# Performance work log

Measured on AMD Instinct MI355X. Metric: run time of the kernel, lower is better.

Reference implementation:

```python
import jax, jax.numpy as jnp
import numpy as np

L = 10   # lattice side (hardcoded self.length)
K = 3    # kernel_size -> half_k = 1 wrap padding
FN = 4   # filter_num
B = 262144


def setup_inputs() -> dict:
    key = jax.random.key(0)
    k1, k2, k3, k4, k5 = jax.random.split(key, 5)
    v = jax.random.normal(k1, (B, L * L), dtype=jnp.float32)
    # torch default init scale ~ 1/sqrt(fan_in)
    conv_w = jax.random.normal(k2, (FN, 1, K, K), dtype=jnp.float32) / 3.0
    conv_b = jax.random.normal(k3, (FN,), dtype=jnp.float32) * 0.1
    deconv_w = jax.random.normal(k4, (FN, 1, 2, 2), dtype=jnp.float32) / 4.0
    deconv_b = jax.random.normal(k5, (1,), dtype=jnp.float32) * 0.1
    data = jnp.zeros((1,), dtype=jnp.int32)  # unused positional arg of log_psi
    return {"v": v, "conv_w": conv_w, "conv_b": conv_b,
            "deconv_w": deconv_w, "deconv_b": deconv_b, "data": data}


def _log_psi(v, conv_w, conv_b, deconv_w, deconv_b):
    b = v.shape[0]
    x = v.reshape(b, 1, L, L)
    # handmade_padding == periodic (wrap) pad of width half_k=1 on both spatial axes
    x = jnp.pad(x, ((0, 0), (0, 0), (1, 1), (1, 1)), mode="wrap")  # [B,1,12,12]
    # Conv2d(1, FN, 3), VALID -> [B,FN,10,10]
    y = jax.lax.conv_general_dilated(
        x, conv_w, window_strides=(1, 1), padding="VALID",
        dimension_numbers=("NCHW", "OIHW", "NCHW"))
    y = y + conv_b[None, :, None, None]
    # MaxPool2d(2,2): non-overlapping 2x2 -> [B,FN,5,5]
    y = y.reshape(b, FN, L // 2, 2, L // 2, 2).max(axis=(3, 5))
    # ConvTranspose2d(FN,1,kernel=2,stride=2): each input pixel -> disjoint 2x2 block
    # torch weight layout [in=FN, out=1, 2, 2]
    z = jnp.einsum("bcij,cokl->boikjl", y, deconv_w).reshape(b, 1, L, L)
    z = z + deconv_b[None, :, None, None]
    sign_z = jnp.sign(z)
    abs_z = z * sign_z
    sign_prod = sign_z.reshape(b, -1).prod(axis=1)        # scalar per sample
    log_sum = jnp.log(abs_z).reshape(b, -1).sum(axis=1)   # scalar per sample
    return sign_prod, log_sum


def reference(v, conv_w, conv_b, deconv_w, deconv_b, data):
    return _log_psi(v, conv_w, conv_b, deconv_w, deconv_b)
```

## Files before the change

### kernel.cpp

```cpp
#include <hip/hip_runtime.h>
#include <math.h>


#define SREAD(x) __int_as_float(__builtin_amdgcn_readfirstlane(__float_as_int(x)))

__device__ __forceinline__ void gload16(const float* g, float* l) {
    __builtin_amdgcn_global_load_lds(
        (const __attribute__((address_space(1))) void*)g,
        (__attribute__((address_space(3))) void*)l, 16, 0, 0);
}
__device__ __forceinline__ void gload4(const float* g, float* l) {
    __builtin_amdgcn_global_load_lds(
        (const __attribute__((address_space(1))) void*)g,
        (__attribute__((address_space(3))) void*)l, 4, 0, 0);
}

__global__ __launch_bounds__(64) void CNN2D_37495064494620_kernel(
    const float* __restrict__ v,
    const float* __restrict__ cw,
    const float* __restrict__ cb,
    const float* __restrict__ dw,
    const float* __restrict__ db,
    float* __restrict__ out,
    int B)
{
    const int l  = threadIdx.x;
    const int q  = l & 1;
    const int sl = l >> 1;

    __shared__ __align__(16) float sm[3200];

    const float* gbase = v + (size_t)blockIdx.x * 3200;
    #pragma unroll
    for (int k = 0; k < 12; ++k)
        gload16(gbase + k * 256 + l * 4, &sm[k * 256]);
    #pragma unroll
    for (int k = 0; k < 2; ++k)
        gload4(gbase + 3072 + k * 64 + l, &sm[3072 + k * 64]);

    float W[4][9];
    #pragma unroll
    for (int f = 0; f < 4; ++f)
        #pragma unroll
        for (int t = 0; t < 9; ++t)
            W[f][t] = SREAD(cw[f * 9 + t]);
    float Cb[4];
    #pragma unroll
    for (int f = 0; f < 4; ++f) Cb[f] = SREAD(cb[f]);
    float Dw[4][4];
    #pragma unroll
    for (int f = 0; f < 4; ++f)
        #pragma unroll
        for (int t = 0; t < 4; ++t)
            Dw[f][t] = SREAD(dw[f * 4 + t]);
    const float Db = SREAD(db[0]);

    __syncthreads();

    const float* my = sm + sl * 100;

    unsigned sbits = 0u;
    float l2 = 0.0f;

    #pragma unroll
    for (int i = 0; i < 5; ++i) {
        const int r1 = 2 * i + q;
        const int r0 = (i == 0) ? (q ? 0 : 9) : (2 * i - 1 + q);
        const int r2 = (i == 4) ? (q ? 0 : 9) : (2 * i + 1 + q);

        float R[3][10];
        #pragma unroll
        for (int t = 0; t < 5; ++t) {
            float2 x0 = *(const float2*)(my + r0 * 10 + 2 * t);
            float2 x1 = *(const float2*)(my + r1 * 10 + 2 * t);
            float2 x2 = *(const float2*)(my + r2 * 10 + 2 * t);
            R[0][2 * t] = x0.x; R[0][2 * t + 1] = x0.y;
            R[1][2 * t] = x1.x; R[1][2 * t + 1] = x1.y;
            R[2][2 * t] = x2.x; R[2][2 * t + 1] = x2.y;
        }

        float M[5][4];
        #pragma unroll
        for (int j = 0; j < 5; ++j) {
            float a0[4], a1[4];
            #pragma unroll
            for (int f = 0; f < 4; ++f) { a0[f] = Cb[f]; a1[f] = Cb[f]; }
            #pragma unroll
            for (int kr = 0; kr < 3; ++kr) {
                #pragma unroll
                for (int kc = 0; kc < 3; ++kc) {
                    const int cc0 = (2 * j + kc + 9) % 10;
                    const int cc1 = (2 * j + 1 + kc + 9) % 10;
                    const float x0 = R[kr][cc0];
                    const float x1 = R[kr][cc1];
                    const int t = kr * 3 + kc;
                    #pragma unroll
                    for (int f = 0; f < 4; ++f) {
                        a0[f] = fmaf(x0, W[f][t], a0[f]);
                        a1[f] = fmaf(x1, W[f][t], a1[f]);
                    }
                }
            }
            #pragma unroll
            for (int f = 0; f < 4; ++f)
                M[j][f] = fmaxf(a0[f], a1[f]);
        }

        float P[5][4];
        #pragma unroll
        for (int j = 0; j < 5; ++j)
            #pragma unroll
            for (int f = 0; f < 4; ++f)
                P[j][f] = fmaxf(M[j][f], __shfl_xor(M[j][f], 1));

        #pragma unroll
        for (int j = 0; j < 5; ++j) {
            float z[4];
            #pragma unroll
            for (int kl = 0; kl < 4; ++kl) {
                float zz = Db;
                #pragma unroll
                for (int f = 0; f < 4; ++f)
                    zz = fmaf(P[j][f], Dw[f][kl], zz);
                z[kl] = zz;
                sbits ^= __float_as_uint(zz);
            }
            l2 += __log2f(fabsf(z[0] * z[1])) + __log2f(fabsf(z[2] * z[3]));
        }
    }

    const int s = blockIdx.x * 32 + sl;
    const float val = q ? (l2 * 0.69314718055994531f)
                        : ((sbits & 0x80000000u) ? -1.0f : 1.0f);
    out[q * B + s] = val;
}

extern "C" void kernel_launch(void* const* d_in, const int* in_sizes, int n_in,
                              void* d_out, int out_size, void* d_ws, size_t ws_size,
                              hipStream_t stream) {
    const float* v  = (const float*)d_in[0];
    const float* cw = (const float*)d_in[1];
    const float* cb = (const float*)d_in[2];
    const float* dw = (const float*)d_in[3];
    const float* db = (const float*)d_in[4];
    float* out = (float*)d_out;

    const int B = in_sizes[0] / 100;
    const int grid = B / 32;
    CNN2D_37495064494620_kernel<<<grid, 64, 0, stream>>>(v, cw, cb, dw, db, out, B);
}
```

Measured before the change: 169.3 us.

## Pack conv FMAs into v2f, split deconv across lane pairs, use DPP swaps

The conv accumulation now uses two-wide float vectors so the compiler can emit packed FMA instructions. The transposed-conv work is split between the two lanes of each pair, so each lane computes only two of the four outputs, and the partial sums and sign bits are combined at the end. Lane-pair shuffles are replaced with DPP quad-permute moves. The block grows from 64 to 256 threads covering 128 samples, which adds LDS per block (about 50KB) and may limit occupancy.

```diff
diff --git a/kernel.cpp b/kernel.cpp
--- a/kernel.cpp
+++ b/kernel.cpp
@@ -2,7 +2,16 @@
 #include <math.h>
 
 
+typedef float v2f __attribute__((ext_vector_type(2)));
+
 #define SREAD(x) __int_as_float(__builtin_amdgcn_readfirstlane(__float_as_int(x)))
+
+__device__ __forceinline__ float dpp_swap1_f(float x) {
+    return __int_as_float(__builtin_amdgcn_mov_dpp(__float_as_int(x), 0xB1, 0xF, 0xF, true));
+}
+__device__ __forceinline__ unsigned dpp_swap1_u(unsigned x) {
+    return (unsigned)__builtin_amdgcn_mov_dpp((int)x, 0xB1, 0xF, 0xF, true);
+}
 
 __device__ __forceinline__ void gload16(const float* g, float* l) {
     __builtin_amdgcn_global_load_lds(
@@ -15,7 +24,7 @@
         (__attribute__((address_space(3))) void*)l, 4, 0, 0);
 }
 
-__global__ __launch_bounds__(64) void CNN2D_37495064494620_kernel(
+__global__ __launch_bounds__(256) void CNN2D_37495064494620_kernel(
     const float* __restrict__ v,
     const float* __restrict__ cw,
     const float* __restrict__ cb,
@@ -24,29 +33,35 @@
     float* __restrict__ out,
     int B)
 {
-    const int l  = threadIdx.x;
-    const int q  = l & 1;
-    const int sl = l >> 1;
+    const int tid = threadIdx.x;
+    const int q   = tid & 1;
+    const int sl  = tid >> 1;
 
-    __shared__ __align__(16) float sm[3200];
+    __shared__ __align__(16) float sm[12800];
 
-    const float* gbase = v + (size_t)blockIdx.x * 3200;
+    const float* gbase = v + (size_t)blockIdx.x * 12800;
+    const int widx = tid >> 6;
     #pragma unroll
     for (int k = 0; k < 12; ++k)
-        gload16(gbase + k * 256 + l * 4, &sm[k * 256]);
+        gload16(gbase + k * 1024 + tid * 4, &sm[k * 1024 + widx * 256]);
     #pragma unroll
     for (int k = 0; k < 2; ++k)
-        gload4(gbase + 3072 + k * 64 + l, &sm[3072 + k * 64]);
+        gload4(gbase + 12288 + k * 256 + tid, &sm[12288 + k * 256 + widx * 64]);
 
-    float W[4][9];
+    float Wf[4][9];
     #pragma unroll
     for (int f = 0; f < 4; ++f)
         #pragma unroll
         for (int t = 0; t < 9; ++t)
-            W[f][t] = SREAD(cw[f * 9 + t]);
-    float Cb[4];
+            Wf[f][t] = SREAD(cw[f * 9 + t]);
+    v2f W2[9][2];
     #pragma unroll
-    for (int f = 0; f < 4; ++f) Cb[f] = SREAD(cb[f]);
+    for (int t = 0; t < 9; ++t) {
+        W2[t][0] = (v2f){Wf[0][t], Wf[1][t]};
+        W2[t][1] = (v2f){Wf[2][t], Wf[3][t]};
+    }
+    const v2f Cb2[2] = { (v2f){SREAD(cb[0]), SREAD(cb[1])},
+                         (v2f){SREAD(cb[2]), SREAD(cb[3])} };
     float Dw[4][4];
     #pragma unroll
     for (int f = 0; f < 4; ++f)
@@ -54,6 +69,11 @@
         for (int t = 0; t < 4; ++t)
             Dw[f][t] = SREAD(dw[f * 4 + t]);
     const float Db = SREAD(db[0]);
+
+    v2f Dq[4];
+    #pragma unroll
+    for (int f = 0; f < 4; ++f)
+        Dq[f] = (v2f){ q ? Dw[f][2] : Dw[f][0], q ? Dw[f][3] : Dw[f][1] };
 
     __syncthreads();
 
@@ -79,57 +99,48 @@
             R[2][2 * t] = x2.x; R[2][2 * t + 1] = x2.y;
         }
 
-        float M[5][4];
         #pragma unroll
         for (int j = 0; j < 5; ++j) {
-            float a0[4], a1[4];
-            #pragma unroll
-            for (int f = 0; f < 4; ++f) { a0[f] = Cb[f]; a1[f] = Cb[f]; }
+            v2f a0[2] = {Cb2[0], Cb2[1]};
+            v2f a1[2] = {Cb2[0], Cb2[1]};
             #pragma unroll
             for (int kr = 0; kr < 3; ++kr) {
                 #pragma unroll
                 for (int kc = 0; kc < 3; ++kc) {
                     const int cc0 = (2 * j + kc + 9) % 10;
                     const int cc1 = (2 * j + 1 + kc + 9) % 10;
-                    const float x0 = R[kr][cc0];
-                    const float x1 = R[kr][cc1];
                     const int t = kr * 3 + kc;
-                    #pragma unroll
-                    for (int f = 0; f < 4; ++f) {
-                        a0[f] = fmaf(x0, W[f][t], a0[f]);
-                        a1[f] = fmaf(x1, W[f][t], a1[f]);
-                    }
+                    const v2f x0 = (v2f){R[kr][cc0], R[kr][cc0]};
+                    const v2f x1 = (v2f){R[kr][cc1], R[kr][cc1]};
+                    a0[0] = __builtin_elementwise_fma(x0, W2[t][0], a0[0]);
+                    a0[1] = __builtin_elementwise_fma(x0, W2[t][1], a0[1]);
+                    a1[0] = __builtin_elementwise_fma(x1, W2[t][0], a1[0]);
+                    a1[1] = __builtin_elementwise_fma(x1, W2[t][1], a1[1]);
                 }
             }
+            const v2f m0 = __builtin_elementwise_max(a0[0], a1[0]);
+            const v2f m1 = __builtin_elementwise_max(a0[1], a1[1]);
+            float P[4];
+            P[0] = fmaxf(m0.x, dpp_swap1_f(m0.x));
+            P[1] = fmaxf(m0.y, dpp_swap1_f(m0.y));
+            P[2] = fmaxf(m1.x, dpp_swap1_f(m1.x));
+            P[3] = fmaxf(m1.y, dpp_swap1_f(m1.y));
+
+            v2f z2 = (v2f){Db, Db};
             #pragma unroll
-            for (int f = 0; f < 4; ++f)
-                M[j][f] = fmaxf(a0[f], a1[f]);
-        }
-
-        float P[5][4];
-        #pragma unroll
-        for (int j = 0; j < 5; ++j)
-            #pragma unroll
-            for (int f = 0; f < 4; ++f)
-                P[j][f] = fmaxf(M[j][f], __shfl_xor(M[j][f], 1));
-
-        #pragma unroll
-        for (int j = 0; j < 5; ++j) {
-            float z[4];
-            #pragma unroll
-            for (int kl = 0; kl < 4; ++kl) {
-                float zz = Db;
-                #pragma unroll
-                for (int f = 0; f < 4; ++f)
-                    zz = fmaf(P[j][f], Dw[f][kl], zz);
-                z[kl] = zz;
-                sbits ^= __float_as_uint(zz);
+            for (int f = 0; f < 4; ++f) {
+                const v2f pf = (v2f){P[f], P[f]};
+                z2 = __builtin_elementwise_fma(pf, Dq[f], z2);
             }
-            l2 += __log2f(fabsf(z[0] * z[1])) + __log2f(fabsf(z[2] * z[3]));
+            sbits ^= __float_as_uint(z2.x) ^ __float_as_uint(z2.y);
+            l2 += __log2f(fabsf(z2.x * z2.y));
         }
     }
 
-    const int s = blockIdx.x * 32 + sl;
+    l2 = l2 + dpp_swap1_f(l2);
+    sbits = sbits ^ dpp_swap1_u(sbits);
+
+    const int s = blockIdx.x * 128 + sl;
     const float val = q ? (l2 * 0.69314718055994531f)
                         : ((sbits & 0x80000000u) ? -1.0f : 1.0f);
     out[q * B + s] = val;
@@ -146,6 +157,6 @@
     float* out = (float*)d_out;
 
     const int B = in_sizes[0] / 100;
-    const int grid = B / 32;
-    CNN2D_37495064494620_kernel<<<grid, 64, 0, stream>>>(v, cw, cb, dw, db, out, B);
+    const int grid = B / 128;
+    CNN2D_37495064494620_kernel<<<grid, 256, 0, stream>>>(v, cw, cb, dw, db, out, B);
 }
```

New measurement: 168.7 us. About the same (-0.3%).
